# Kernel tuning notes

Measured on AMD Instinct MI355X. Metric: run time of the kernel, lower is better.

## Reference

```python
import jax, jax.numpy as jnp
import numpy as np
import math

LATENT = 4
LAYERS = 2
B = 524288


def _apply_1q_batched(state, U, wire):
    # state: (B,2,2,2,2), U: (B,2,2) per-sample gate on `wire`
    s = jnp.moveaxis(state, wire + 1, -1)
    s = jnp.einsum('bij,b...j->b...i', U, s)
    return jnp.moveaxis(s, -1, wire + 1)


def _apply_1q_shared(state, U, wire):
    # state: (B,2,2,2,2), U: (2,2) shared gate on `wire`
    s = jnp.moveaxis(state, wire + 1, -1)
    s = jnp.einsum('ij,b...j->b...i', U, s)
    return jnp.moveaxis(s, -1, wire + 1)


def _cnot(state, control, target):
    s = jnp.moveaxis(state, (control + 1, target + 1), (-2, -1))
    s = jnp.concatenate([s[..., :1, :], s[..., 1:, ::-1]], axis=-2)
    return jnp.moveaxis(s, (-2, -1), (control + 1, target + 1))


def _rot_matrix(phi, theta, omega):
    # PennyLane Rot(phi, theta, omega) = RZ(omega) RY(theta) RZ(phi)
    ct = jnp.cos(theta / 2).astype(jnp.complex64)
    st = jnp.sin(theta / 2).astype(jnp.complex64)
    ep = jnp.exp(-0.5j * (phi + omega).astype(jnp.complex64))
    em = jnp.exp(-0.5j * (phi - omega).astype(jnp.complex64))
    return jnp.stack([
        jnp.stack([ep * ct, -jnp.conj(em) * st]),
        jnp.stack([em * st, jnp.conj(ep) * ct]),
    ])


def _circuit(angles, weights):
    # angles: (B,4) RY rotation angles; weights: (LAYERS,4,3)
    Bn = angles.shape[0]
    state = jnp.zeros((Bn, 2, 2, 2, 2), jnp.complex64).at[:, 0, 0, 0, 0].set(1.0)
    # per-sample RY encoding
    for w in range(LATENT):
        th = angles[:, w] / 2
        c, s = jnp.cos(th), jnp.sin(th)
        U = jnp.stack([jnp.stack([c, -s], -1), jnp.stack([s, c], -1)], -2)
        state = _apply_1q_batched(state, U.astype(jnp.complex64), w)
    for l in range(LAYERS):
        for w in range(LATENT):
            U = _rot_matrix(weights[l, w, 0], weights[l, w, 1], weights[l, w, 2])
            state = _apply_1q_shared(state, U, w)
        for w in range(LATENT):
            state = _cnot(state, w, (w + 1) % LATENT)
    probs = jnp.abs(state) ** 2  # (B,2,2,2,2) float32
    zv = jnp.array([1.0, -1.0], jnp.float32)
    exps = jnp.stack([
        jnp.einsum('bpqrs,p->b', probs, zv),
        jnp.einsum('bpqrs,q->b', probs, zv),
        jnp.einsum('bpqrs,r->b', probs, zv),
        jnp.einsum('bpqrs,s->b', probs, zv),
    ], axis=-1)  # (B,4)
    return exps


def setup_inputs() -> dict:
    key = jax.random.key(0)
    k1, k2, k3, k4 = jax.random.split(key, 4)
    z = jax.random.normal(k1, (B, LATENT), jnp.float32)
    q_weights = jax.random.normal(k2, (LAYERS, LATENT, 3), jnp.float32)
    scale = jnp.asarray(math.pi, jnp.float32)
    lim = 1.0 / math.sqrt(LATENT)
    W = jax.random.uniform(k3, (LATENT, LATENT), jnp.float32, -lim, lim)
    b = jax.random.uniform(k4, (LATENT,), jnp.float32, -lim, lim)
    return {"z": z, "scale": scale, "q_weights": q_weights, "W": W, "b": b}


def reference(z, scale, q_weights, W, b):
    angles = jnp.tanh(z) * scale          # (B,4)
    zq = _circuit(angles, q_weights)      # (B,4) PauliZ expectations
    return zq @ W.T + b                   # Linear(4,4)
```

## Files before the change

### kernel.cpp

```cpp
#include <hip/hip_runtime.h>
#include <hip/hip_bf16.h>
#include <math.h>


typedef __attribute__((ext_vector_type(8))) short bf16x8;
typedef __attribute__((ext_vector_type(4))) float f32x4;

__device__ __forceinline__ float2 qb_cmul(float2 a, float2 b) {
    return make_float2(a.x * b.x - a.y * b.y, a.x * b.y + a.y * b.x);
}

__device__ __forceinline__ unsigned qb_pk(float a, float b) {
    union { __hip_bfloat16 h; unsigned short u; } A, B;
    A.h = __float2bfloat16(a);
    B.h = __float2bfloat16(b);
    return (unsigned)A.u | ((unsigned)B.u << 16);
}

__global__ void __launch_bounds__(256) qb_fused(
    const float* __restrict__ z, const float* __restrict__ scale,
    const float* __restrict__ qw, const float* __restrict__ W,
    const float* __restrict__ bias, float* __restrict__ out, int Bn)
{
    __shared__ __align__(16) char shpool[53248];
    __shared__ __align__(16) float sC[81 * 4];
    __shared__ __align__(16) unsigned short sGbH[4][96];
    __shared__ __align__(16) unsigned short sGbL[4][96];

    float  (*sTrig)[6]  = (float(*)[6])  (shpool);
    float2  *sU         = (float2*)      (shpool + 192);
    float2 (*sV1)[16]   = (float2(*)[16])(shpool + 448);
    float2 (*sU2)[16]   = (float2(*)[16])(shpool + 2496);
    float  (*Vr)[16]    = (float(*)[16]) (shpool + 4544);
    float  (*Vi)[16]    = (float(*)[16]) (shpool + 5568);
    float4  *sM         = (float4*)      (shpool + 6592);
    unsigned short *Eb  = (unsigned short*)shpool;

    const int tid = threadIdx.x;

    if (tid < 24) {
        const int g = tid / 3, which = tid % 3;
        const float phi = qw[g * 3 + 0], th = qw[g * 3 + 1], om = qw[g * 3 + 2];
        const float ang = (which == 0) ? 0.5f * th
                        : (which == 1) ? 0.5f * (phi + om)
                                       : 0.5f * (phi - om);
        float sn, cs;
        __sincosf(ang, &sn, &cs);
        sTrig[g][2 * which + 0] = cs;
        sTrig[g][2 * which + 1] = sn;
    }
    __syncthreads();

    if (tid < 32) {
        const int l = tid >> 4, w = (tid >> 2) & 3, r = (tid >> 1) & 1, c = tid & 1;
        const int g = l * 4 + w;
        const float ct  = sTrig[g][0], st  = sTrig[g][1];
        const float epr = sTrig[g][2], epi = -sTrig[g][3];
        const float emr = sTrig[g][4], emi = -sTrig[g][5];
        float re, im;
        if (r == 0 && c == 0)      { re =  epr * ct; im =  epi * ct; }
        else if (r == 0)           { re = -emr * st; im =  emi * st; }
        else if (c == 0)           { re =  emr * st; im =  emi * st; }
        else                       { re =  epr * ct; im = -epi * ct; }
        sU[((l * 4 + w) * 2 + r) * 2 + c] = make_float2(re, im);
    }
    __syncthreads();

    const int vi = tid >> 4, vk = tid & 15;
    {
        const int i0 = (vi >> 3) & 1, i1 = (vi >> 2) & 1, i2 = (vi >> 1) & 1, i3 = vi & 1;
        const int k0 = (vk >> 3) & 1, k1 = (vk >> 2) & 1, k2 = (vk >> 1) & 1, k3 = vk & 1;
        int b0 = i0, b1 = i1, b2 = i2, b3 = i3;
        b1 ^= b0; b2 ^= b1; b3 ^= b2; b0 ^= b3;
        const int sig = (b0 << 3) | (b1 << 2) | (b2 << 1) | b3;
        const float2 e1 = qb_cmul(qb_cmul(sU[(0*4+0)*4 + i0*2 + k0], sU[(0*4+1)*4 + i1*2 + k1]),
                                  qb_cmul(sU[(0*4+2)*4 + i2*2 + k2], sU[(0*4+3)*4 + i3*2 + k3]));
        const float2 e2 = qb_cmul(qb_cmul(sU[(1*4+0)*4 + i0*2 + k0], sU[(1*4+1)*4 + i1*2 + k1]),
                                  qb_cmul(sU[(1*4+2)*4 + i2*2 + k2], sU[(1*4+3)*4 + i3*2 + k3]));
        sV1[sig][vk] = e1;
        sU2[vi][vk]  = e2;
    }
    __syncthreads();

    {
        const int i0 = (vi >> 3) & 1, i1 = (vi >> 2) & 1, i2 = (vi >> 1) & 1, i3 = vi & 1;
        int b0 = i0, b1 = i1, b2 = i2, b3 = i3;
        b1 ^= b0; b2 ^= b1; b3 ^= b2; b0 ^= b3;
        const int sig = (b0 << 3) | (b1 << 2) | (b2 << 1) | b3;
        float accr = 0.f, acci = 0.f;
        #pragma unroll
        for (int m = 0; m < 16; ++m) {
            const float2 u = sU2[vi][m];
            const float2 v = sV1[m][vk];
            accr += u.x * v.x - u.y * v.y;
            acci += u.x * v.y + u.y * v.x;
        }
        Vr[sig][vk] = accr;
        Vi[sig][vk] = acci;
    }
    __syncthreads();

    {
        const int k = tid >> 4, kp = tid & 15;
        float m0 = 0.f, m1 = 0.f, m2 = 0.f, m3 = 0.f;
        #pragma unroll
        for (int i = 0; i < 16; ++i) {
            const float pr = Vr[i][k] * Vr[i][kp] + Vi[i][k] * Vi[i][kp];
            m0 += ((i >> 3) & 1) ? -pr : pr;
            m1 += ((i >> 2) & 1) ? -pr : pr;
            m2 += ((i >> 1) & 1) ? -pr : pr;
            m3 += ( i       & 1) ? -pr : pr;
        }
        sM[tid] = make_float4(m0, m1, m2, m3);
    }
    __syncthreads();

    if (tid < 81) {
        const int mm[4] = { tid / 27, (tid / 9) % 3, (tid / 3) % 3, tid % 3 };
        float h0 = 0.f, h1 = 0.f, h2 = 0.f, h3 = 0.f;
        #pragma unroll
        for (int t16 = 0; t16 < 16; ++t16) {
            int k = 0, kp = 0;
            float sgn = 0.0625f;
            #pragma unroll
            for (int w = 0; w < 4; ++w) {
                const int b = (t16 >> (3 - w)) & 1;
                int kw, kpw;
                if (mm[w] == 2) { kw = b; kpw = 1 - b; }
                else            { kw = b; kpw = b; if (mm[w] == 1 && b) sgn = -sgn; }
                k  |= kw  << (3 - w);
                kp |= kpw << (3 - w);
            }
            const float4 mv = sM[k * 16 + kp];
            h0 += sgn * mv.x; h1 += sgn * mv.y; h2 += sgn * mv.z; h3 += sgn * mv.w;
        }
        #pragma unroll
        for (int j = 0; j < 4; ++j) {
            sC[tid * 4 + j] = W[j * 4 + 0] * h0 + W[j * 4 + 1] * h1 +
                              W[j * 4 + 2] * h2 + W[j * 4 + 3] * h3;
        }
    }
    __syncthreads();

    if (tid < 96) {
        #pragma unroll
        for (int j = 0; j < 4; ++j) {
            float gv = (tid < 81) ? sC[tid * 4 + j] : 0.0f;
            union { __hip_bfloat16 h; unsigned short u; } H, L;
            H.h = __float2bfloat16(gv);
            float hi = __bfloat162float(H.h);
            L.h = __float2bfloat16(gv - hi);
            sGbH[j][tid] = H.u;
            sGbL[j][tid] = L.u;
        }
    }
    __syncthreads();

    const int lane = tid & 63, wid = tid >> 6;
    const int fm = lane & 15, koct = lane >> 4;

    bf16x8 aH0 = {0,0,0,0,0,0,0,0}, aH1 = aH0, aH2 = aH0;
    bf16x8 aL0 = aH0, aL1 = aH0, aL2 = aH0;
    if (fm < 4) {
        aH0 = *reinterpret_cast<const bf16x8*>(&sGbH[fm][ 0 + koct * 8]);
        aH1 = *reinterpret_cast<const bf16x8*>(&sGbH[fm][32 + koct * 8]);
        aH2 = *reinterpret_cast<const bf16x8*>(&sGbH[fm][64 + koct * 8]);
        aL0 = *reinterpret_cast<const bf16x8*>(&sGbL[fm][ 0 + koct * 8]);
        aL1 = *reinterpret_cast<const bf16x8*>(&sGbL[fm][32 + koct * 8]);
        aL2 = *reinterpret_cast<const bf16x8*>(&sGbL[fm][64 + koct * 8]);
    }
    const float sc = scale[0];
    f32x4 biasv;
    biasv[0] = bias[0]; biasv[1] = bias[1]; biasv[2] = bias[2]; biasv[3] = bias[3];

    unsigned short* ebw = Eb + (wid * 64) * 104;
    const int base = blockIdx.x * 1024 + wid * 256;

    #pragma unroll 1
    for (int sp = 0; sp < 4; ++sp) {
        const int s0 = base + sp * 64;
        const int myIdx = s0 + lane;
        const float4 zv = (myIdx < Bn) ? reinterpret_cast<const float4*>(z)[myIdx]
                                       : make_float4(0.f, 0.f, 0.f, 0.f);
        const float zz[4] = { zv.x, zv.y, zv.z, zv.w };
        float c[4], sn[4];
        #pragma unroll
        for (int w = 0; w < 4; ++w) {
            const float e = __expf(2.0f * zz[w]);
            const float t = 1.0f - __fdividef(2.0f, e + 1.0f);
            __sincosf(t * sc, &sn[w], &c[w]);
        }
        const float e01[9] = { 1.0f,  c[1],        sn[1],
                               c[0],  c[0]*c[1],   c[0]*sn[1],
                               sn[0], sn[0]*c[1],  sn[0]*sn[1] };
        const float e23[9] = { 1.0f,  c[3],        sn[3],
                               c[2],  c[2]*c[3],   c[2]*sn[3],
                               sn[2], sn[2]*c[3],  sn[2]*sn[3] };

        uint4* rowv = reinterpret_cast<uint4*>(ebw + lane * 104);
        #pragma unroll
        for (int oct = 0; oct < 10; ++oct) {
            float E[8];
            #pragma unroll
            for (int e = 0; e < 8; ++e) {
                const int mm = oct * 8 + e;
                E[e] = e01[mm / 9] * e23[mm % 9];
            }
            rowv[oct] = make_uint4(qb_pk(E[0], E[1]), qb_pk(E[2], E[3]),
                                   qb_pk(E[4], E[5]), qb_pk(E[6], E[7]));
        }
        rowv[10] = make_uint4(qb_pk(e01[8] * e23[8], 0.f), 0u, 0u, 0u);
        rowv[11] = make_uint4(0u, 0u, 0u, 0u);

        #pragma unroll
        for (int p = 0; p < 4; ++p) {
            const unsigned short* br = ebw + (p * 16 + fm) * 104;
            const bf16x8 b0v = *reinterpret_cast<const bf16x8*>(br +  0 + koct * 8);
            const bf16x8 b1v = *reinterpret_cast<const bf16x8*>(br + 32 + koct * 8);
            const bf16x8 b2v = *reinterpret_cast<const bf16x8*>(br + 64 + koct * 8);
            f32x4 acc = biasv;
            acc = __builtin_amdgcn_mfma_f32_16x16x32_bf16(aH0, b0v, acc, 0, 0, 0);
            acc = __builtin_amdgcn_mfma_f32_16x16x32_bf16(aH1, b1v, acc, 0, 0, 0);
            acc = __builtin_amdgcn_mfma_f32_16x16x32_bf16(aH2, b2v, acc, 0, 0, 0);
            acc = __builtin_amdgcn_mfma_f32_16x16x32_bf16(aL0, b0v, acc, 0, 0, 0);
            acc = __builtin_amdgcn_mfma_f32_16x16x32_bf16(aL1, b1v, acc, 0, 0, 0);
            acc = __builtin_amdgcn_mfma_f32_16x16x32_bf16(aL2, b2v, acc, 0, 0, 0);
            if (koct == 0) {
                const int oidx = s0 + p * 16 + lane;
                if (oidx < Bn)
                    reinterpret_cast<float4*>(out)[oidx] =
                        make_float4(acc[0], acc[1], acc[2], acc[3]);
            }
        }
        asm volatile("" ::: "memory");
    }
}

extern "C" void kernel_launch(void* const* d_in, const int* in_sizes, int n_in,
                              void* d_out, int out_size, void* d_ws, size_t ws_size,
                              hipStream_t stream) {
    const float* z  = (const float*)d_in[0];
    const float* sc = (const float*)d_in[1];
    const float* qw = (const float*)d_in[2];
    const float* W  = (const float*)d_in[3];
    const float* bb = (const float*)d_in[4];
    float* out = (float*)d_out;

    const int Bn = in_sizes[0] / 4;
    const int blocks = (Bn + 1023) / 1024;

    hipLaunchKernelGGL(qb_fused, dim3(blocks), dim3(256), 0, stream,
                       z, sc, qw, W, bb, out, Bn);
}
```

Measured before the change: 17.35 us.

## Prefetch z at kernel start, unroll sample loop, split MFMA accumulators

All four float4 loads of z per thread are issued at kernel entry, so their latency overlaps the shared-memory coefficient setup phase. The loop over four sub-batches becomes a fully unrolled lambda. The hi and lo MFMA chains now accumulate into two independent registers that are summed at the end, which shortens the dependent MFMA chain. This costs more registers and code size, and it changes the summation order slightly.

After: 19.26 us. +11.0%, slower.

```diff
diff --git a/kernel.cpp b/kernel.cpp
--- a/kernel.cpp
+++ b/kernel.cpp
@@ -37,6 +37,16 @@
     unsigned short *Eb  = (unsigned short*)shpool;
 
     const int tid = threadIdx.x;
+    const int lane = tid & 63, wid = tid >> 6;
+    const int base = blockIdx.x * 1024 + wid * 256;
+
+    const float4 zzero = make_float4(0.f, 0.f, 0.f, 0.f);
+    const int i0_ = base + 0 * 64 + lane, i1_ = base + 1 * 64 + lane;
+    const int i2_ = base + 2 * 64 + lane, i3_ = base + 3 * 64 + lane;
+    const float4 zp0 = (i0_ < Bn) ? reinterpret_cast<const float4*>(z)[i0_] : zzero;
+    const float4 zp1 = (i1_ < Bn) ? reinterpret_cast<const float4*>(z)[i1_] : zzero;
+    const float4 zp2 = (i2_ < Bn) ? reinterpret_cast<const float4*>(z)[i2_] : zzero;
+    const float4 zp3 = (i3_ < Bn) ? reinterpret_cast<const float4*>(z)[i3_] : zzero;
 
     if (tid < 24) {
         const int g = tid / 3, which = tid % 3;
@@ -156,7 +166,6 @@
     }
     __syncthreads();
 
-    const int lane = tid & 63, wid = tid >> 6;
     const int fm = lane & 15, koct = lane >> 4;
 
     bf16x8 aH0 = {0,0,0,0,0,0,0,0}, aH1 = aH0, aH2 = aH0;
@@ -174,14 +183,8 @@
     biasv[0] = bias[0]; biasv[1] = bias[1]; biasv[2] = bias[2]; biasv[3] = bias[3];
 
     unsigned short* ebw = Eb + (wid * 64) * 104;
-    const int base = blockIdx.x * 1024 + wid * 256;
-
-    #pragma unroll 1
-    for (int sp = 0; sp < 4; ++sp) {
-        const int s0 = base + sp * 64;
-        const int myIdx = s0 + lane;
-        const float4 zv = (myIdx < Bn) ? reinterpret_cast<const float4*>(z)[myIdx]
-                                       : make_float4(0.f, 0.f, 0.f, 0.f);
+
+    auto dbody = [&](int s0, const float4& zv) {
         const float zz[4] = { zv.x, zv.y, zv.z, zv.w };
         float c[4], sn[4];
         #pragma unroll
@@ -218,22 +221,31 @@
             const bf16x8 b0v = *reinterpret_cast<const bf16x8*>(br +  0 + koct * 8);
             const bf16x8 b1v = *reinterpret_cast<const bf16x8*>(br + 32 + koct * 8);
             const bf16x8 b2v = *reinterpret_cast<const bf16x8*>(br + 64 + koct * 8);
-            f32x4 acc = biasv;
-            acc = __builtin_amdgcn_mfma_f32_16x16x32_bf16(aH0, b0v, acc, 0, 0, 0);
-            acc = __builtin_amdgcn_mfma_f32_16x16x32_bf16(aH1, b1v, acc, 0, 0, 0);
-            acc = __builtin_amdgcn_mfma_f32_16x16x32_bf16(aH2, b2v, acc, 0, 0, 0);
-            acc = __builtin_amdgcn_mfma_f32_16x16x32_bf16(aL0, b0v, acc, 0, 0, 0);
-            acc = __builtin_amdgcn_mfma_f32_16x16x32_bf16(aL1, b1v, acc, 0, 0, 0);
-            acc = __builtin_amdgcn_mfma_f32_16x16x32_bf16(aL2, b2v, acc, 0, 0, 0);
+            f32x4 accH = biasv;
+            f32x4 accL; accL[0] = accL[1] = accL[2] = accL[3] = 0.0f;
+            accH = __builtin_amdgcn_mfma_f32_16x16x32_bf16(aH0, b0v, accH, 0, 0, 0);
+            accL = __builtin_amdgcn_mfma_f32_16x16x32_bf16(aL0, b0v, accL, 0, 0, 0);
+            accH = __builtin_amdgcn_mfma_f32_16x16x32_bf16(aH1, b1v, accH, 0, 0, 0);
+            accL = __builtin_amdgcn_mfma_f32_16x16x32_bf16(aL1, b1v, accL, 0, 0, 0);
+            accH = __builtin_amdgcn_mfma_f32_16x16x32_bf16(aH2, b2v, accH, 0, 0, 0);
+            accL = __builtin_amdgcn_mfma_f32_16x16x32_bf16(aL2, b2v, accL, 0, 0, 0);
             if (koct == 0) {
                 const int oidx = s0 + p * 16 + lane;
                 if (oidx < Bn)
                     reinterpret_cast<float4*>(out)[oidx] =
-                        make_float4(acc[0], acc[1], acc[2], acc[3]);
+                        make_float4(accH[0] + accL[0], accH[1] + accL[1],
+                                    accH[2] + accL[2], accH[3] + accL[3]);
             }
         }
-        asm volatile("" ::: "memory");
-    }
+    };
+
+    dbody(base + 0 * 64, zp0);
+    asm volatile("" ::: "memory");
+    dbody(base + 1 * 64, zp1);
+    asm volatile("" ::: "memory");
+    dbody(base + 2 * 64, zp2);
+    asm volatile("" ::: "memory");
+    dbody(base + 3 * 64, zp3);
 }
 
 extern "C" void kernel_launch(void* const* d_in, const int* in_sizes, int n_in,
```
